# Performance work log

Measured on AMD Instinct MI355X. Metric: run time of the kernel, lower is better.

The kernel has to match this reference:

```python
import jax, jax.numpy as jnp
import numpy as np

# Offsets from init_kwargs: short- and long-range affinities along x and y.
OFFSETS = ((-1, 0), (0, -1), (-2, 0), (0, -2), (-4, 0), (0, -4), (-8, 0), (0, -8))
B, C, H, W = 1, 1, 4096, 4096
N_LABELS = 64


def setup_inputs() -> dict:
    key = jax.random.key(0)
    # Integer instance labels stored as float (module runs conv on float dtype).
    seg = jax.random.randint(key, (B, C, H, W), 0, N_LABELS).astype(jnp.float32)
    return {"segmentation": seg}


def _shift(x, ox, oy):
    """Zero-padded shift: out[i,j] = x[i+ox, j+oy] (0 outside).

    Exactly reproduces F.conv2d with the 3x3 kernel (-1 at center, +1 at the
    sign-determined corner), dilation=max(1,|off|), padding=max(1,|off|):
    the conv output equals shift(x, ox, oy) - x.
    """
    ax, ay = abs(ox), abs(oy)
    p = jnp.pad(x, ((0, 0), (0, 0), (ax, ax), (ay, ay)))
    Hh, Ww = x.shape[-2], x.shape[-1]
    return p[:, :, ax + ox:ax + ox + Hh, ay + oy:ay + oy + Ww]


def reference(segmentation) -> jnp.ndarray:
    seg = segmentation  # [B,1,H,W]
    affs = []
    for ox, oy in OFFSETS:  # small fixed offset list -> static unroll
        grad = _shift(seg, ox, oy) - seg          # spatial gradient
        aff = jnp.where(grad == 0, jnp.ones_like(grad), jnp.zeros_like(grad))
        affs.append(aff)
    out = jnp.stack(affs, axis=0)  # [O, B, 1, H, W]
    # torch .squeeze(1).squeeze(1) with B=1 -> [O, H, W]
    return out[:, 0, 0]
```

## Files before the change

### kernel.cpp

```cpp
#include <hip/hip_runtime.h>
#include <hip/hip_bf16.h>


#define IMG_H 4096
#define IMG_W 4096
#define BAND  16

typedef float floatx4 __attribute__((ext_vector_type(4)));

__device__ __forceinline__ float4 ld4(const float* p) { return *(const float4*)p; }

__device__ __forceinline__ void st4_nt(float* p, float4 v) {
    floatx4 x = { v.x, v.y, v.z, v.w };
    __builtin_nontemporal_store(x, (floatx4*)p);
}

__device__ __forceinline__ float4 eq4(float4 a, float4 b) {
    return make_float4(a.x == b.x ? 1.0f : 0.0f,
                       a.y == b.y ? 1.0f : 0.0f,
                       a.z == b.z ? 1.0f : 0.0f,
                       a.w == b.w ? 1.0f : 0.0f);
}

__global__ __launch_bounds__(256) void GetAffs_83416854823610_kernel(
        const float* __restrict__ seg, float* __restrict__ out) {
    const int jq = blockIdx.x * 256 + threadIdx.x;
    const int j  = jq << 2;
    const int i0 = blockIdx.y * BAND;
    const float4 zero4 = make_float4(0.f, 0.f, 0.f, 0.f);

    float4 hist[8];
#pragma unroll
    for (int k = 0; k < 8; ++k) {
        const int r = i0 - 8 + k;
        hist[k] = (r >= 0) ? ld4(seg + (size_t)r * IMG_W + j) : zero4;
    }

    const size_t HW = (size_t)IMG_H * IMG_W;

#pragma unroll
    for (int u = 0; u < BAND; ++u) {
        const int i = i0 + u;
        const float* row = seg + (size_t)i * IMG_W;
        const float4 c  = ld4(row + j);
        const float4 l1 = (j >= 4) ? ld4(row + j - 4) : zero4;
        const float4 l2 = (j >= 8) ? ld4(row + j - 8) : zero4;

        const float4 v1 = hist[(u + 7) & 7];
        const float4 v2 = hist[(u + 6) & 7];
        const float4 v4 = hist[(u + 4) & 7];
        const float4 v8 = hist[u & 7];

        const float4 h1 = make_float4(l1.w, c.x, c.y, c.z);
        const float4 h2 = make_float4(l1.z, l1.w, c.x, c.y);
        const float4 h4 = l1;
        const float4 h8 = l2;

        const size_t base = (size_t)i * IMG_W + (size_t)j;
        st4_nt(out + 0 * HW + base, eq4(v1, c));
        st4_nt(out + 1 * HW + base, eq4(h1, c));
        st4_nt(out + 2 * HW + base, eq4(v2, c));
        st4_nt(out + 3 * HW + base, eq4(h2, c));
        st4_nt(out + 4 * HW + base, eq4(v4, c));
        st4_nt(out + 5 * HW + base, eq4(h4, c));
        st4_nt(out + 6 * HW + base, eq4(v8, c));
        st4_nt(out + 7 * HW + base, eq4(h8, c));

        hist[u & 7] = c;
    }
}

extern "C" void kernel_launch(void* const* d_in, const int* in_sizes, int n_in,
                              void* d_out, int out_size, void* d_ws, size_t ws_size,
                              hipStream_t stream) {
    const float* seg = (const float*)d_in[0];
    float* out = (float*)d_out;
    dim3 grid((IMG_W / 4) / 256, IMG_H / BAND);
    dim3 block(256);
    GetAffs_83416854823610_kernel<<<grid, block, 0, stream>>>(seg, out);
}
```

Baseline: 578.0 us.

## Split vertical and horizontal affinities into separate blocks; use plain stores

Adds a z-dimension of size 2 to the grid so vertical-offset channels and horizontal-offset channels are computed by different blocks, which doubles the block count and halves per-thread store work. It also replaces nontemporal stores with ordinary vector stores. The cost is that the input rows are read twice, once per block type, and the cache behaviour of the 512 MB output write changes with the store type.

```diff
diff --git a/kernel.cpp b/kernel.cpp
--- a/kernel.cpp
+++ b/kernel.cpp
@@ -6,14 +6,8 @@
 #define IMG_W 4096
 #define BAND  16
 
-typedef float floatx4 __attribute__((ext_vector_type(4)));
-
 __device__ __forceinline__ float4 ld4(const float* p) { return *(const float4*)p; }
-
-__device__ __forceinline__ void st4_nt(float* p, float4 v) {
-    floatx4 x = { v.x, v.y, v.z, v.w };
-    __builtin_nontemporal_store(x, (floatx4*)p);
-}
+__device__ __forceinline__ void st4(float* p, float4 v) { *(float4*)p = v; }
 
 __device__ __forceinline__ float4 eq4(float4 a, float4 b) {
     return make_float4(a.x == b.x ? 1.0f : 0.0f,
@@ -28,45 +22,48 @@
     const int j  = jq << 2;
     const int i0 = blockIdx.y * BAND;
     const float4 zero4 = make_float4(0.f, 0.f, 0.f, 0.f);
-
-    float4 hist[8];
-#pragma unroll
-    for (int k = 0; k < 8; ++k) {
-        const int r = i0 - 8 + k;
-        hist[k] = (r >= 0) ? ld4(seg + (size_t)r * IMG_W + j) : zero4;
-    }
-
     const size_t HW = (size_t)IMG_H * IMG_W;
 
+    if (blockIdx.z == 0) {
+        float4 hist[8];
 #pragma unroll
-    for (int u = 0; u < BAND; ++u) {
-        const int i = i0 + u;
-        const float* row = seg + (size_t)i * IMG_W;
-        const float4 c  = ld4(row + j);
-        const float4 l1 = (j >= 4) ? ld4(row + j - 4) : zero4;
-        const float4 l2 = (j >= 8) ? ld4(row + j - 8) : zero4;
-
-        const float4 v1 = hist[(u + 7) & 7];
-        const float4 v2 = hist[(u + 6) & 7];
-        const float4 v4 = hist[(u + 4) & 7];
-        const float4 v8 = hist[u & 7];
-
-        const float4 h1 = make_float4(l1.w, c.x, c.y, c.z);
-        const float4 h2 = make_float4(l1.z, l1.w, c.x, c.y);
-        const float4 h4 = l1;
-        const float4 h8 = l2;
-
-        const size_t base = (size_t)i * IMG_W + (size_t)j;
-        st4_nt(out + 0 * HW + base, eq4(v1, c));
-        st4_nt(out + 1 * HW + base, eq4(h1, c));
-        st4_nt(out + 2 * HW + base, eq4(v2, c));
-        st4_nt(out + 3 * HW + base, eq4(h2, c));
-        st4_nt(out + 4 * HW + base, eq4(v4, c));
-        st4_nt(out + 5 * HW + base, eq4(h4, c));
-        st4_nt(out + 6 * HW + base, eq4(v8, c));
-        st4_nt(out + 7 * HW + base, eq4(h8, c));
-
-        hist[u & 7] = c;
+        for (int k = 0; k < 8; ++k) {
+            const int r = i0 - 8 + k;
+            hist[k] = (r >= 0) ? ld4(seg + (size_t)r * IMG_W + j) : zero4;
+        }
+#pragma unroll
+        for (int u = 0; u < BAND; ++u) {
+            const int i = i0 + u;
+            const float4 c = ld4(seg + (size_t)i * IMG_W + j);
+            const float4 v1 = hist[(u + 7) & 7];
+            const float4 v2 = hist[(u + 6) & 7];
+            const float4 v4 = hist[(u + 4) & 7];
+            const float4 v8 = hist[u & 7];
+            const size_t base = (size_t)i * IMG_W + (size_t)j;
+            st4(out + 0 * HW + base, eq4(v1, c));
+            st4(out + 2 * HW + base, eq4(v2, c));
+            st4(out + 4 * HW + base, eq4(v4, c));
+            st4(out + 6 * HW + base, eq4(v8, c));
+            hist[u & 7] = c;
+        }
+    } else {
+#pragma unroll
+        for (int u = 0; u < BAND; ++u) {
+            const int i = i0 + u;
+            const float* row = seg + (size_t)i * IMG_W;
+            const float4 c  = ld4(row + j);
+            const float4 l1 = (j >= 4) ? ld4(row + j - 4) : zero4;
+            const float4 l2 = (j >= 8) ? ld4(row + j - 8) : zero4;
+            const float4 h1 = make_float4(l1.w, c.x, c.y, c.z);
+            const float4 h2 = make_float4(l1.z, l1.w, c.x, c.y);
+            const float4 h4 = l1;
+            const float4 h8 = l2;
+            const size_t base = (size_t)i * IMG_W + (size_t)j;
+            st4(out + 1 * HW + base, eq4(h1, c));
+            st4(out + 3 * HW + base, eq4(h2, c));
+            st4(out + 5 * HW + base, eq4(h4, c));
+            st4(out + 7 * HW + base, eq4(h8, c));
+        }
     }
 }
 
@@ -75,7 +72,7 @@
                               hipStream_t stream) {
     const float* seg = (const float*)d_in[0];
     float* out = (float*)d_out;
-    dim3 grid((IMG_W / 4) / 256, IMG_H / BAND);
+    dim3 grid((IMG_W / 4) / 256, IMG_H / BAND, 2);
     dim3 block(256);
     GetAffs_83416854823610_kernel<<<grid, block, 0, stream>>>(seg, out);
 }
```

Result: slower. 601.9 us (+4.1%).

## Split affinity planes across grid z dimension, one plane per block

Applied to the files above, without the earlier changes.

Restructures the kernel so each block computes only one of the eight output planes, selected by blockIdx.z through templated per-offset code. Each block then writes to a single contiguous output plane rather than eight strided ones, and the grid has eight times as many blocks. The cost is that every plane re-reads the input (eight times the input traffic, though it should mostly hit in cache), and the register-held row history used to reuse vertical neighbours is dropped.

```diff
diff --git a/kernel.cpp b/kernel.cpp
--- a/kernel.cpp
+++ b/kernel.cpp
@@ -22,51 +22,50 @@
                        a.w == b.w ? 1.0f : 0.0f);
 }
 
-__global__ __launch_bounds__(256) void GetAffs_83416854823610_kernel(
-        const float* __restrict__ seg, float* __restrict__ out) {
-    const int jq = blockIdx.x * 256 + threadIdx.x;
-    const int j  = jq << 2;
-    const int i0 = blockIdx.y * BAND;
+template <int OX, int OY>
+__device__ __forceinline__ void do_plane(const float* __restrict__ seg,
+                                         float* __restrict__ po,
+                                         int i0, int j) {
     const float4 zero4 = make_float4(0.f, 0.f, 0.f, 0.f);
-
-    float4 hist[8];
-#pragma unroll
-    for (int k = 0; k < 8; ++k) {
-        const int r = i0 - 8 + k;
-        hist[k] = (r >= 0) ? ld4(seg + (size_t)r * IMG_W + j) : zero4;
-    }
-
-    const size_t HW = (size_t)IMG_H * IMG_W;
-
 #pragma unroll
     for (int u = 0; u < BAND; ++u) {
         const int i = i0 + u;
         const float* row = seg + (size_t)i * IMG_W;
-        const float4 c  = ld4(row + j);
-        const float4 l1 = (j >= 4) ? ld4(row + j - 4) : zero4;
-        const float4 l2 = (j >= 8) ? ld4(row + j - 8) : zero4;
+        const float4 c = ld4(row + j);
+        float4 nb;
+        if (OY == 0) {
+            nb = (i + OX >= 0) ? ld4(seg + (size_t)(i + OX) * IMG_W + j) : zero4;
+        } else if (OY == -1) {
+            const float4 l1 = (j >= 4) ? ld4(row + j - 4) : zero4;
+            nb = make_float4(l1.w, c.x, c.y, c.z);
+        } else if (OY == -2) {
+            const float4 l1 = (j >= 4) ? ld4(row + j - 4) : zero4;
+            nb = make_float4(l1.z, l1.w, c.x, c.y);
+        } else if (OY == -4) {
+            nb = (j >= 4) ? ld4(row + j - 4) : zero4;
+        } else {
+            nb = (j >= 8) ? ld4(row + j - 8) : zero4;
+        }
+        st4_nt(po + (size_t)i * IMG_W + j, eq4(nb, c));
+    }
+}
 
-        const float4 v1 = hist[(u + 7) & 7];
-        const float4 v2 = hist[(u + 6) & 7];
-        const float4 v4 = hist[(u + 4) & 7];
-        const float4 v8 = hist[u & 7];
+__global__ __launch_bounds__(256) void GetAffs_83416854823610_kernel(
+        const float* __restrict__ seg, float* __restrict__ out) {
+    const int j  = (blockIdx.x * 256 + threadIdx.x) << 2;
+    const int i0 = blockIdx.y * BAND;
+    const size_t HW = (size_t)IMG_H * IMG_W;
+    float* po = out + (size_t)blockIdx.z * HW;
 
-        const float4 h1 = make_float4(l1.w, c.x, c.y, c.z);
-        const float4 h2 = make_float4(l1.z, l1.w, c.x, c.y);
-        const float4 h4 = l1;
-        const float4 h8 = l2;
-
-        const size_t base = (size_t)i * IMG_W + (size_t)j;
-        st4_nt(out + 0 * HW + base, eq4(v1, c));
-        st4_nt(out + 1 * HW + base, eq4(h1, c));
-        st4_nt(out + 2 * HW + base, eq4(v2, c));
-        st4_nt(out + 3 * HW + base, eq4(h2, c));
-        st4_nt(out + 4 * HW + base, eq4(v4, c));
-        st4_nt(out + 5 * HW + base, eq4(h4, c));
-        st4_nt(out + 6 * HW + base, eq4(v8, c));
-        st4_nt(out + 7 * HW + base, eq4(h8, c));
-
-        hist[u & 7] = c;
+    switch (blockIdx.z) {
+        case 0: do_plane<-1,  0>(seg, po, i0, j); break;
+        case 1: do_plane< 0, -1>(seg, po, i0, j); break;
+        case 2: do_plane<-2,  0>(seg, po, i0, j); break;
+        case 3: do_plane< 0, -2>(seg, po, i0, j); break;
+        case 4: do_plane<-4,  0>(seg, po, i0, j); break;
+        case 5: do_plane< 0, -4>(seg, po, i0, j); break;
+        case 6: do_plane<-8,  0>(seg, po, i0, j); break;
+        case 7: do_plane< 0, -8>(seg, po, i0, j); break;
     }
 }
 
@@ -75,7 +74,7 @@
                               hipStream_t stream) {
     const float* seg = (const float*)d_in[0];
     float* out = (float*)d_out;
-    dim3 grid((IMG_W / 4) / 256, IMG_H / BAND);
+    dim3 grid((IMG_W / 4) / 256, IMG_H / BAND, 8);
     dim3 block(256);
     GetAffs_83416854823610_kernel<<<grid, block, 0, stream>>>(seg, out);
 }
```

After: 610.6 us. 1.06x slower.
